# Kernel tuning notes

Hardware: AMD Instinct MI355X
Metric: run time of the kernel (lower is better)

## Reference

```python
import jax, jax.numpy as jnp
import numpy as np

EMBEDDING_DIM = 128
CODEBOOK_SIZE = 8192
COMMITMENT_COST = 0.25


def setup_inputs() -> dict:
    key = jax.random.key(0)
    k1, k2 = jax.random.split(key)
    inputs = jax.random.normal(k1, (8, 2048, EMBEDDING_DIM), dtype=jnp.float32)
    embeddings = jax.random.normal(k2, (EMBEDDING_DIM, CODEBOOK_SIZE), dtype=jnp.float32)
    return {"inputs": inputs, "embeddings": embeddings}


def reference(inputs, embeddings):
    # inputs: [B, T, D]; embeddings: [D, K]
    B, T, D = inputs.shape
    K = embeddings.shape[1]
    flat = inputs.reshape(-1, D)                      # [N, D]
    sim = flat @ embeddings                           # [N, K]
    dists = (jnp.sum(flat * flat, axis=1, keepdims=True)
             - 2.0 * sim
             + jnp.sum(embeddings * embeddings, axis=0, keepdims=True))
    idx_flat = jnp.argmax(-dists, axis=1)             # [N], matches tf.argmax(-d)
    encodings = jax.nn.one_hot(idx_flat, K, dtype=inputs.dtype)  # [N, K]
    encoding_indices = idx_flat.reshape(B, T)
    quantized = jnp.take(embeddings.T, encoding_indices, axis=0)  # [B, T, D]
    e_latent_loss = jnp.mean((jax.lax.stop_gradient(quantized) - inputs) ** 2)
    q_latent_loss = jnp.mean((quantized - jax.lax.stop_gradient(inputs)) ** 2)
    loss = q_latent_loss + COMMITMENT_COST * e_latent_loss
    quantized = inputs + jax.lax.stop_gradient(quantized - inputs)  # straight-through
    return quantized, encodings, encoding_indices, loss
```

## Files before the change

kernel.cpp:

```cpp
#include <hip/hip_runtime.h>

#define D 128
#define K 8192
#define N 16384
#define BM 64
#define BN 256
#define NCH (K / BN)
#define THREADS 512
#define CAND_CAP 2944
#define DELTA 0.5f
#define RMIN_INIT 0xFF800000u

typedef __attribute__((ext_vector_type(4))) float f32x4;
typedef __attribute__((ext_vector_type(16))) float f32x16;
typedef __attribute__((ext_vector_type(8))) short short8;

__device__ __forceinline__ unsigned short f2bf(float f) {
    unsigned int b = __float_as_uint(f);
    return (unsigned short)((b + 0x7FFFu + ((b >> 16) & 1u)) >> 16);
}
__device__ __forceinline__ unsigned int fsort(float f) {
    unsigned int b = __float_as_uint(f);
    return b ^ ((unsigned int)((int)b >> 31) | 0x80000000u);
}
__device__ __forceinline__ float funsort(unsigned int u) {
    return __uint_as_float((u & 0x80000000u) ? (u ^ 0x80000000u) : ~u);
}

__device__ __forceinline__ void lds_barrier() {
    asm volatile("s_waitcnt lgkmcnt(0)" ::: "memory");
    __builtin_amdgcn_s_barrier();
}

__global__ __launch_bounds__(256) void prep_kernel(const float* __restrict__ E,
        unsigned short* __restrict__ e1t, unsigned short* __restrict__ augt,
        float* __restrict__ e2t, float* __restrict__ enorm) {
    __shared__ float esum[8][32];
    const int t = threadIdx.x;
    const int kl = t & 31, dg = t >> 5;
    const int k = blockIdx.x * 32 + kl;
    float s = 0.f;
    __align__(16) unsigned short tmpb[16];
    __align__(16) float tmpf[16];
#pragma unroll
    for (int j = 0; j < 16; ++j) {
        float v = E[(size_t)(dg * 16 + j) * K + k];
        s += v * v;
        tmpb[j] = f2bf(v);
        tmpf[j] = v;
    }
    *(f32x4*)(e1t + (size_t)k * D + dg * 16) = *(const f32x4*)tmpb;
    *(f32x4*)(e1t + (size_t)k * D + dg * 16 + 8) = *(const f32x4*)(tmpb + 8);
    if (e2t) {
#pragma unroll
        for (int q = 0; q < 4; ++q)
            *(f32x4*)(e2t + (size_t)k * D + dg * 16 + 4 * q) = *(const f32x4*)(tmpf + 4 * q);
    }
    esum[dg][kl] = s;
    __syncthreads();
    if (t < 32) {
        float e = 0.f;
#pragma unroll
        for (int g = 0; g < 8; ++g) e += esum[g][t];
        const int kk = blockIdx.x * 32 + t;
        enorm[kk] = e;
        unsigned short hi = f2bf(e);
        float hif = __uint_as_float((unsigned int)hi << 16);
        unsigned short lo = f2bf(e - hif);
        __align__(16) unsigned short av[8] = {hi, lo, 0, 0, 0, 0, 0, 0};
        *(f32x4*)(augt + (size_t)kk * 8) = *(const f32x4*)av;
    }
}

template<int E2T>
__global__ __launch_bounds__(THREADS, 2) void main_kernel(
        const float* __restrict__ X, const float* __restrict__ E,
        const unsigned short* __restrict__ e1t, const unsigned short* __restrict__ augt,
        const float* __restrict__ e2t, const float* __restrict__ enorm,
        float* __restrict__ out, float* __restrict__ partials) {
    __shared__ __align__(16) unsigned short b_s[2][BN * D];
    __shared__ __align__(16) unsigned short aug_s[2][BN * 8];
    __shared__ unsigned long long cand[CAND_CAP];
    __shared__ unsigned long long best[BM];
    __shared__ unsigned int rmin[BM];
    __shared__ int candn;

    const int t = threadIdx.x;
    const int wid = t >> 6, l = t & 63;
    const int l31 = l & 31, lh = l >> 5;
    const int wm = wid >> 2, wn = wid & 3;
    const int rowbase = blockIdx.x * BM;

    float* qout = out;
    float* enc = out + (size_t)N * D;
    float* idxout = enc + (size_t)N * K;

    if (t < BM) { rmin[t] = RMIN_INIT; best[t] = ~0ull; }
    if (t == 0) candn = 0;

    short8 afr[8];
    {
        const int row = rowbase + wm * 32 + l31;
#pragma unroll
        for (int ks = 0; ks < 8; ++ks) {
            const float* xp = X + (size_t)row * D + ks * 16 + lh * 8;
            f32x4 v0 = *(const f32x4*)xp;
            f32x4 v1 = *(const f32x4*)(xp + 4);
            short8 a;
            a[0] = (short)f2bf(-2.f * v0[0]); a[1] = (short)f2bf(-2.f * v0[1]);
            a[2] = (short)f2bf(-2.f * v0[2]); a[3] = (short)f2bf(-2.f * v0[3]);
            a[4] = (short)f2bf(-2.f * v1[0]); a[5] = (short)f2bf(-2.f * v1[1]);
            a[6] = (short)f2bf(-2.f * v1[2]); a[7] = (short)f2bf(-2.f * v1[3]);
            afr[ks] = a;
        }
    }
    short8 a_aug;
    {
        const short one = (short)0x3F80;
        a_aug[0] = (lh == 0) ? one : (short)0;
        a_aug[1] = (lh == 0) ? one : (short)0;
        a_aug[2] = 0; a_aug[3] = 0; a_aug[4] = 0;
        a_aug[5] = 0; a_aug[6] = 0; a_aug[7] = 0;
    }

    f32x4 sreg[8];
    f32x4 avreg;
    {
        const f32x4* gs = (const f32x4*)e1t;
#pragma unroll
        for (int i = 0; i < 8; ++i) sreg[i] = gs[t + THREADS * i];
        if (t < 256) avreg = *(const f32x4*)(augt + (size_t)t * 8);
#pragma unroll
        for (int i = 0; i < 8; ++i) {
            int unit = t + THREADS * i;
            int c = unit >> 4, slot = unit & 15;
            *(f32x4*)((char*)&b_s[0][0] + c * 256 + ((slot ^ (c & 15)) << 4)) = sreg[i];
        }
        if (t < 256) *(f32x4*)((char*)&aug_s[0][0] + t * 16) = avreg;
    }

    int cur = 0;
    for (int ch = 0; ch < NCH; ++ch) {
        if (ch + 1 < NCH) {
            const f32x4* gs = (const f32x4*)(e1t + (size_t)(ch + 1) * BN * D);
#pragma unroll
            for (int i = 0; i < 8; ++i) sreg[i] = gs[t + THREADS * i];
            if (t < 256) avreg = *(const f32x4*)(augt + (size_t)(ch + 1) * BN * 8 + t * 8);
        }
        lds_barrier();

        const int chcol = ch * BN;

        {
            const f32x4 z = {0.f, 0.f, 0.f, 0.f};
#pragma unroll
            for (int i = 0; i < 8; ++i) {
                int unit = t + THREADS * i;
                int row = unit >> 6, cu = unit & 63;
                __builtin_nontemporal_store(z,
                    (f32x4*)(enc + (size_t)(rowbase + row) * K + chcol + cu * 4));
            }
        }

        float thrv[16];
#pragma unroll
        for (int q = 0; q < 4; ++q) {
            const int base = wm * 32 + 4 * lh + 8 * q;
            uint4 rv = *(const uint4*)&rmin[base];
            thrv[4 * q + 0] = funsort(rv.x);
            thrv[4 * q + 1] = funsort(rv.y);
            thrv[4 * q + 2] = funsort(rv.z);
            thrv[4 * q + 3] = funsort(rv.w);
        }

        f32x16 acc[2];
#pragma unroll
        for (int nf = 0; nf < 2; ++nf)
#pragma unroll
            for (int r = 0; r < 16; ++r) acc[nf][r] = 0.f;

#pragma unroll
        for (int ks = 0; ks < 8; ++ks) {
            short8 bf[2];
#pragma unroll
            for (int nf = 0; nf < 2; ++nf) {
                int c = wn * 64 + nf * 32 + l31;
                int slot = ks * 2 + lh;
                bf[nf] = *(const short8*)((const char*)&b_s[cur][0] + c * 256 + ((slot ^ (c & 15)) << 4));
            }
#pragma unroll
            for (int nf = 0; nf < 2; ++nf)
                acc[nf] = __builtin_amdgcn_mfma_f32_32x32x16_bf16(afr[ks], bf[nf], acc[nf], 0, 0, 0);
        }
#pragma unroll
        for (int nf = 0; nf < 2; ++nf) {
            const int c = wn * 64 + nf * 32 + l31;
            short8 ba = {0, 0, 0, 0, 0, 0, 0, 0};
            if (lh == 0) ba = *(const short8*)((const char*)&aug_s[cur][0] + c * 16);
            acc[nf] = __builtin_amdgcn_mfma_f32_32x32x16_bf16(a_aug, ba, acc[nf], 0, 0, 0);
        }

        float cmin[16];
#pragma unroll
        for (int r = 0; r < 16; ++r) cmin[r] = fminf(acc[0][r], acc[1][r]);
#pragma unroll
        for (int m = 1; m <= 16; m <<= 1)
#pragma unroll
            for (int r = 0; r < 16; ++r)
                cmin[r] = fminf(cmin[r], __shfl_xor(cmin[r], m, 64));

#pragma unroll
        for (int r = 0; r < 16; ++r) {
            const int ro = wm * 32 + 4 * lh + 8 * (r >> 2) + (r & 3);
            const float te = fminf(thrv[r], cmin[r]) + DELTA;
#pragma unroll
            for (int nf = 0; nf < 2; ++nf) {
                if (acc[nf][r] < te) {
                    const int col = chcol + wn * 64 + nf * 32 + l31;
                    int ci = atomicAdd(&candn, 1);
                    if (ci < CAND_CAP)
                        cand[ci] = ((unsigned long long)fsort(acc[nf][r]) << 32) |
                                   ((unsigned long long)ro << 13) | (unsigned)col;
                }
            }
            if (l31 == 0 && cmin[r] < thrv[r])
                atomicMin(&rmin[ro], fsort(cmin[r]));
        }

        if (ch + 1 < NCH) {
#pragma unroll
            for (int i = 0; i < 8; ++i) {
                int unit = t + THREADS * i;
                int c = unit >> 4, slot = unit & 15;
                *(f32x4*)((char*)&b_s[cur ^ 1][0] + c * 256 + ((slot ^ (c & 15)) << 4)) = sreg[i];
            }
            if (t < 256) *(f32x4*)((char*)&aug_s[cur ^ 1][0] + t * 16) = avreg;
        }
        cur ^= 1;
    }

    __syncthreads();

    {
        int n = candn; if (n > CAND_CAP) n = CAND_CAP;
        for (int i = wid; i < n; i += 8) {
            const unsigned long long e = cand[i];
            const float dta = funsort((unsigned int)(e >> 32));
            const int ro = (int)((e >> 13) & 63u);
            const int col = (int)(e & 8191u);
            if (dta < funsort(rmin[ro]) + DELTA) {
                const int row = rowbase + ro;
                float x0 = X[(size_t)row * D + l];
                float x1 = X[(size_t)row * D + 64 + l];
                float e0, e1;
                if (E2T) {
                    e0 = e2t[(size_t)col * D + l];
                    e1 = e2t[(size_t)col * D + 64 + l];
                } else {
                    e0 = E[(size_t)l * K + col];
                    e1 = E[(size_t)(l + 64) * K + col];
                }
                float s = x0 * e0 + x1 * e1;
#pragma unroll
                for (int m = 1; m <= 32; m <<= 1) s += __shfl_xor(s, m, 64);
                if (l == 0) {
                    float dtx = enorm[col] - 2.f * s;
                    atomicMin(&best[ro],
                        ((unsigned long long)fsort(dtx) << 32) | (unsigned)col);
                }
            }
        }
    }
    __syncthreads();

    float* red = (float*)&b_s[0][0];
    if (t < BM) {
        const int k = (int)(best[t] & 8191ull);
        idxout[rowbase + t] = (float)k;
        __builtin_nontemporal_store(1.0f, &enc[(size_t)(rowbase + t) * K + k]);
    }

    const int rr = t >> 3, sL = t & 7;
    const int row = rowbase + rr;
    const int kb = (int)(best[rr] & 8191ull);
    float part = 0.f;
#pragma unroll
    for (int j = 0; j < 4; ++j) {
        const int d0 = sL * 16 + 4 * j;
        f32x4 xv = *(const f32x4*)(X + (size_t)row * D + d0);
        f32x4 ev;
        if (E2T) {
            ev = *(const f32x4*)(e2t + (size_t)kb * D + d0);
        } else {
#pragma unroll
            for (int u = 0; u < 4; ++u) ev[u] = E[(size_t)(d0 + u) * K + kb];
        }
        f32x4 qv;
#pragma unroll
        for (int u = 0; u < 4; ++u) {
            float df = ev[u] - xv[u];
            qv[u] = xv[u] + df;
            part += df * df;
        }
        *(f32x4*)(qout + (size_t)row * D + d0) = qv;
    }
    red[t] = part;
    __syncthreads();
#pragma unroll
    for (int off = THREADS / 2; off > 0; off >>= 1) {
        if (t < off) red[t] += red[t + off];
        __syncthreads();
    }
    if (t == 0) partials[blockIdx.x] = red[0];
}

__global__ __launch_bounds__(256) void loss_kernel(const float* __restrict__ partials,
                                                   float* __restrict__ out) {
    __shared__ float red[256];
    const int t = threadIdx.x;
    red[t] = partials[t];
    __syncthreads();
    for (int off = 128; off > 0; off >>= 1) {
        if (t < off) red[t] += red[t + off];
        __syncthreads();
    }
    if (t == 0) {
        float mean = red[0] / (float)((size_t)N * D);
        out[(size_t)N * D + (size_t)N * K + N] = mean + 0.25f * mean;
    }
}

extern "C" void kernel_launch(void* const* d_in, const int* in_sizes, int n_in,
                              void* d_out, int out_size, void* d_ws, size_t ws_size,
                              hipStream_t stream) {
    const float* X = (const float*)d_in[0];
    const float* E = (const float*)d_in[1];
    float* out = (float*)d_out;
    char* ws = (char*)d_ws;

    const size_t E1T_B = (size_t)K * D * 2;
    const size_t AUG_B = (size_t)K * 8 * 2;
    const size_t E2T_B = (size_t)K * D * 4;
    const bool use_e2t = ws_size >= E1T_B + AUG_B + E2T_B + 64 * 1024;

    unsigned short* e1t = (unsigned short*)ws;
    unsigned short* augt = (unsigned short*)(ws + E1T_B);
    float* e2t; float* enorm; float* partials;
    if (use_e2t) {
        e2t = (float*)(ws + E1T_B + AUG_B);
        enorm = (float*)(ws + E1T_B + AUG_B + E2T_B);
        partials = enorm + K;
    } else {
        e2t = nullptr;
        enorm = (float*)(ws + E1T_B + AUG_B);
        partials = enorm + K;
    }

    hipLaunchKernelGGL(prep_kernel, dim3(K / 32), dim3(256), 0, stream,
                       E, e1t, augt, e2t, enorm);
    if (use_e2t)
        hipLaunchKernelGGL((main_kernel<1>), dim3(N / BM), dim3(THREADS), 0, stream,
                           X, E, e1t, augt, e2t, enorm, out, partials);
    else
        hipLaunchKernelGGL((main_kernel<0>), dim3(N / BM), dim3(THREADS), 0, stream,
                           X, E, e1t, augt, e2t, enorm, out, partials);
    hipLaunchKernelGGL(loss_kernel, dim3(1), dim3(256), 0, stream, partials, out);
}
```

Baseline: 194.6 us.

## Shrink tiles to 32x128 and batch candidate filtering across four chunks

Halves the row and column tile sizes and uses 256 threads in four waves, so each wave computes one 32x32 MFMA tile per chunk. It saves distances for four chunks in registers, then does the shuffle min-reduction and the threshold/candidate pass once per group. This cuts the per-chunk reduction, atomics and threshold reads, and doubles the grid to 512 blocks for better occupancy. The costs are more register pressure, twice the codebook reloads across blocks, and a smaller candidate buffer, which risks overflow.

```diff
diff --git a/kernel.cpp b/kernel.cpp
--- a/kernel.cpp
+++ b/kernel.cpp
@@ -3,11 +3,12 @@
 #define D 128
 #define K 8192
 #define N 16384
-#define BM 64
-#define BN 256
+#define BM 32
+#define BN 128
 #define NCH (K / BN)
-#define THREADS 512
-#define CAND_CAP 2944
+#define GRP 4
+#define THREADS 256
+#define CAND_CAP 1024
 #define DELTA 0.5f
 #define RMIN_INIT 0xFF800000u
 
@@ -88,7 +89,7 @@
     const int t = threadIdx.x;
     const int wid = t >> 6, l = t & 63;
     const int l31 = l & 31, lh = l >> 5;
-    const int wm = wid >> 2, wn = wid & 3;
+    const int wn = wid;
     const int rowbase = blockIdx.x * BM;
 
     float* qout = out;
@@ -100,7 +101,7 @@
 
     short8 afr[8];
     {
-        const int row = rowbase + wm * 32 + l31;
+        const int row = rowbase + l31;
 #pragma unroll
         for (int ks = 0; ks < 8; ++ks) {
             const float* xp = X + (size_t)row * D + ks * 16 + lh * 8;
@@ -129,43 +130,88 @@
         const f32x4* gs = (const f32x4*)e1t;
 #pragma unroll
         for (int i = 0; i < 8; ++i) sreg[i] = gs[t + THREADS * i];
-        if (t < 256) avreg = *(const f32x4*)(augt + (size_t)t * 8);
+        if (t < 128) avreg = *(const f32x4*)(augt + (size_t)t * 8);
 #pragma unroll
         for (int i = 0; i < 8; ++i) {
             int unit = t + THREADS * i;
             int c = unit >> 4, slot = unit & 15;
             *(f32x4*)((char*)&b_s[0][0] + c * 256 + ((slot ^ (c & 15)) << 4)) = sreg[i];
         }
-        if (t < 256) *(f32x4*)((char*)&aug_s[0][0] + t * 16) = avreg;
+        if (t < 128) *(f32x4*)((char*)&aug_s[0][0] + t * 16) = avreg;
     }
 
     int cur = 0;
-    for (int ch = 0; ch < NCH; ++ch) {
-        if (ch + 1 < NCH) {
-            const f32x4* gs = (const f32x4*)(e1t + (size_t)(ch + 1) * BN * D);
-#pragma unroll
-            for (int i = 0; i < 8; ++i) sreg[i] = gs[t + THREADS * i];
-            if (t < 256) avreg = *(const f32x4*)(augt + (size_t)(ch + 1) * BN * 8 + t * 8);
-        }
-        lds_barrier();
-
-        const int chcol = ch * BN;
-
-        {
-            const f32x4 z = {0.f, 0.f, 0.f, 0.f};
-#pragma unroll
-            for (int i = 0; i < 8; ++i) {
-                int unit = t + THREADS * i;
-                int row = unit >> 6, cu = unit & 63;
-                __builtin_nontemporal_store(z,
-                    (f32x4*)(enc + (size_t)(rowbase + row) * K + chcol + cu * 4));
-            }
-        }
+    for (int cg = 0; cg < NCH / GRP; ++cg) {
+        float dsave[GRP][16];
+#pragma unroll
+        for (int g = 0; g < GRP; ++g) {
+            const int ch = cg * GRP + g;
+            if (ch + 1 < NCH) {
+                const f32x4* gs = (const f32x4*)(e1t + (size_t)(ch + 1) * BN * D);
+#pragma unroll
+                for (int i = 0; i < 8; ++i) sreg[i] = gs[t + THREADS * i];
+                if (t < 128) avreg = *(const f32x4*)(augt + (size_t)(ch + 1) * BN * 8 + t * 8);
+            }
+            lds_barrier();
+
+            {
+                const f32x4 z = {0.f, 0.f, 0.f, 0.f};
+#pragma unroll
+                for (int i = 0; i < 4; ++i) {
+                    int unit = t + THREADS * i;
+                    int row = unit >> 5, cu = unit & 31;
+                    __builtin_nontemporal_store(z,
+                        (f32x4*)(enc + (size_t)(rowbase + row) * K + ch * BN + cu * 4));
+                }
+            }
+
+            f32x16 acc;
+#pragma unroll
+            for (int r = 0; r < 16; ++r) acc[r] = 0.f;
+#pragma unroll
+            for (int ks = 0; ks < 8; ++ks) {
+                const int c = wn * 32 + l31;
+                const int slot = ks * 2 + lh;
+                short8 bf = *(const short8*)((const char*)&b_s[cur][0] + c * 256 +
+                                             ((slot ^ (c & 15)) << 4));
+                acc = __builtin_amdgcn_mfma_f32_32x32x16_bf16(afr[ks], bf, acc, 0, 0, 0);
+            }
+            {
+                const int c = wn * 32 + l31;
+                short8 ba = {0, 0, 0, 0, 0, 0, 0, 0};
+                if (lh == 0) ba = *(const short8*)((const char*)&aug_s[cur][0] + c * 16);
+                acc = __builtin_amdgcn_mfma_f32_32x32x16_bf16(a_aug, ba, acc, 0, 0, 0);
+            }
+#pragma unroll
+            for (int r = 0; r < 16; ++r) dsave[g][r] = acc[r];
+
+            if (ch + 1 < NCH) {
+#pragma unroll
+                for (int i = 0; i < 8; ++i) {
+                    int unit = t + THREADS * i;
+                    int c = unit >> 4, slot = unit & 15;
+                    *(f32x4*)((char*)&b_s[cur ^ 1][0] + c * 256 + ((slot ^ (c & 15)) << 4)) = sreg[i];
+                }
+                if (t < 128) *(f32x4*)((char*)&aug_s[cur ^ 1][0] + t * 16) = avreg;
+            }
+            cur ^= 1;
+        }
+
+        float lmin[16];
+#pragma unroll
+        for (int r = 0; r < 16; ++r)
+            lmin[r] = fminf(fminf(dsave[0][r], dsave[1][r]),
+                            fminf(dsave[2][r], dsave[3][r]));
+#pragma unroll
+        for (int m = 1; m <= 16; m <<= 1)
+#pragma unroll
+            for (int r = 0; r < 16; ++r)
+                lmin[r] = fminf(lmin[r], __shfl_xor(lmin[r], m, 64));
 
         float thrv[16];
 #pragma unroll
         for (int q = 0; q < 4; ++q) {
-            const int base = wm * 32 + 4 * lh + 8 * q;
+            const int base = 8 * q + 4 * lh;
             uint4 rv = *(const uint4*)&rmin[base];
             thrv[4 * q + 0] = funsort(rv.x);
             thrv[4 * q + 1] = funsort(rv.y);
@@ -173,77 +219,30 @@
             thrv[4 * q + 3] = funsort(rv.w);
         }
 
-        f32x16 acc[2];
-#pragma unroll
-        for (int nf = 0; nf < 2; ++nf)
-#pragma unroll
-            for (int r = 0; r < 16; ++r) acc[nf][r] = 0.f;
-
-#pragma unroll
-        for (int ks = 0; ks < 8; ++ks) {
-            short8 bf[2];
-#pragma unroll
-            for (int nf = 0; nf < 2; ++nf) {
-                int c = wn * 64 + nf * 32 + l31;
-                int slot = ks * 2 + lh;
-                bf[nf] = *(const short8*)((const char*)&b_s[cur][0] + c * 256 + ((slot ^ (c & 15)) << 4));
-            }
-#pragma unroll
-            for (int nf = 0; nf < 2; ++nf)
-                acc[nf] = __builtin_amdgcn_mfma_f32_32x32x16_bf16(afr[ks], bf[nf], acc[nf], 0, 0, 0);
-        }
-#pragma unroll
-        for (int nf = 0; nf < 2; ++nf) {
-            const int c = wn * 64 + nf * 32 + l31;
-            short8 ba = {0, 0, 0, 0, 0, 0, 0, 0};
-            if (lh == 0) ba = *(const short8*)((const char*)&aug_s[cur][0] + c * 16);
-            acc[nf] = __builtin_amdgcn_mfma_f32_32x32x16_bf16(a_aug, ba, acc[nf], 0, 0, 0);
-        }
-
-        float cmin[16];
-#pragma unroll
-        for (int r = 0; r < 16; ++r) cmin[r] = fminf(acc[0][r], acc[1][r]);
-#pragma unroll
-        for (int m = 1; m <= 16; m <<= 1)
-#pragma unroll
-            for (int r = 0; r < 16; ++r)
-                cmin[r] = fminf(cmin[r], __shfl_xor(cmin[r], m, 64));
-
 #pragma unroll
         for (int r = 0; r < 16; ++r) {
-            const int ro = wm * 32 + 4 * lh + 8 * (r >> 2) + (r & 3);
-            const float te = fminf(thrv[r], cmin[r]) + DELTA;
-#pragma unroll
-            for (int nf = 0; nf < 2; ++nf) {
-                if (acc[nf][r] < te) {
-                    const int col = chcol + wn * 64 + nf * 32 + l31;
+            const int ro = (r & 3) + 8 * (r >> 2) + 4 * lh;
+            const float te = fminf(thrv[r], lmin[r]) + DELTA;
+#pragma unroll
+            for (int g = 0; g < GRP; ++g) {
+                if (dsave[g][r] < te) {
+                    const int col = (cg * GRP + g) * BN + wn * 32 + l31;
                     int ci = atomicAdd(&candn, 1);
                     if (ci < CAND_CAP)
-                        cand[ci] = ((unsigned long long)fsort(acc[nf][r]) << 32) |
+                        cand[ci] = ((unsigned long long)fsort(dsave[g][r]) << 32) |
                                    ((unsigned long long)ro << 13) | (unsigned)col;
                 }
             }
-            if (l31 == 0 && cmin[r] < thrv[r])
-                atomicMin(&rmin[ro], fsort(cmin[r]));
-        }
-
-        if (ch + 1 < NCH) {
-#pragma unroll
-            for (int i = 0; i < 8; ++i) {
-                int unit = t + THREADS * i;
-                int c = unit >> 4, slot = unit & 15;
-                *(f32x4*)((char*)&b_s[cur ^ 1][0] + c * 256 + ((slot ^ (c & 15)) << 4)) = sreg[i];
-            }
-            if (t < 256) *(f32x4*)((char*)&aug_s[cur ^ 1][0] + t * 16) = avreg;
-        }
-        cur ^= 1;
+            if (l31 == 0 && lmin[r] < thrv[r])
+                atomicMin(&rmin[ro], fsort(lmin[r]));
+        }
     }
 
     __syncthreads();
 
     {
         int n = candn; if (n > CAND_CAP) n = CAND_CAP;
-        for (int i = wid; i < n; i += 8) {
+        for (int i = wid; i < n; i += 4) {
             const unsigned long long e = cand[i];
             const float dta = funsort((unsigned int)(e >> 32));
             const int ro = (int)((e >> 13) & 63u);
@@ -318,7 +317,7 @@
                                                    float* __restrict__ out) {
     __shared__ float red[256];
     const int t = threadIdx.x;
-    red[t] = partials[t];
+    red[t] = partials[t] + partials[t + 256];
     __syncthreads();
     for (int off = 128; off > 0; off >>= 1) {
         if (t < off) red[t] += red[t + off];
```

After: 173.1 us. -11.0%, faster.
